# Optimization experiments

Hardware: AMD Instinct MI355X
Metric: run time of the kernel (lower is better)

## Reference

```python
import jax, jax.numpy as jnp
import numpy as np

T = 512        # seq_len
D = 128        # output_dim / trajectory feature dim
H_ENC = 512    # encoder hidden
H_DEC = 512    # decoder hidden
EMB = 256      # embedding size


def _lstm_step(h, c, x, Wi, Wh, bh):
    # flax LSTMCell: input dense has no bias, hidden dense has bias
    z = x @ Wi + h @ Wh + bh              # [4H]
    i, f, g, o = jnp.split(z, 4)
    i = jax.nn.sigmoid(i)
    f = jax.nn.sigmoid(f)
    g = jnp.tanh(g)
    o = jax.nn.sigmoid(o)
    c_new = f * c + i * g
    h_new = o * jnp.tanh(c_new)
    return h_new, c_new


def setup_inputs() -> dict:
    key = jax.random.key(0)
    ks = jax.random.split(key, 12)
    def w(k, shape, fan_in):
        return jax.random.normal(k, shape, dtype=jnp.float32) / np.sqrt(fan_in)
    return {
        "trajectory": jax.random.normal(ks[0], (T, D), dtype=jnp.float32),
        # encoder LSTM
        "enc_Wi": w(ks[1], (D, 4 * H_ENC), D),
        "enc_Wh": w(ks[2], (H_ENC, 4 * H_ENC), H_ENC),
        "enc_bh": jnp.zeros((4 * H_ENC,), jnp.float32),
        # encoder embedding projection
        "enc_emb_W": w(ks[3], (H_ENC, EMB), H_ENC),
        "enc_emb_b": jnp.zeros((EMB,), jnp.float32),
        # decoder initial-hidden projection from embedding
        "dec_init_W": w(ks[4], (EMB, H_DEC), EMB),
        "dec_init_b": jnp.zeros((H_DEC,), jnp.float32),
        # decoder LSTM
        "dec_Wi": w(ks[5], (D, 4 * H_DEC), D),
        "dec_Wh": w(ks[6], (H_DEC, 4 * H_DEC), H_DEC),
        "dec_bh": jnp.zeros((4 * H_DEC,), jnp.float32),
        # per-timestep decoder output Dense (fresh module each loop iter in original)
        "dec_out_W": w(ks[7], (T, H_DEC, D), H_DEC),
        "dec_out_b": jnp.zeros((T, D), jnp.float32),
    }


def reference(trajectory, enc_Wi, enc_Wh, enc_bh, enc_emb_W, enc_emb_b,
              dec_init_W, dec_init_b, dec_Wi, dec_Wh, dec_bh,
              dec_out_W, dec_out_b):
    # ---- Encoder: sequential LSTM over trajectory, zero init carry ----
    def enc_step(carry, x_t):
        h, c = carry
        h, c = _lstm_step(h, c, x_t, enc_Wi, enc_Wh, enc_bh)
        return (h, c), None
    h0 = jnp.zeros((H_ENC,), trajectory.dtype)
    c0 = jnp.zeros((H_ENC,), trajectory.dtype)
    (h, _), _ = jax.lax.scan(enc_step, (h0, c0), trajectory)
    embedding = h @ enc_emb_W + enc_emb_b  # [EMB]

    # per-timestep output Dense weights ----
    def dec_step(carry, wt):
        h, c, x = carry
        Wt, bt = wt
        h, c = _lstm_step(h, c, x, dec_Wi, dec_Wh, dec_bh)
        x = h @ Wt + bt  # flax LSTMCell output y == new h
        return (h, c, x), x
    hd0 = embedding @ dec_init_W + dec_init_b   # [H_DEC]
    cd0 = jnp.zeros((H_DEC,), trajectory.dtype)
    x0 = jnp.zeros((D,), trajectory.dtype)
    _, reconstruction = jax.lax.scan(dec_step, (hd0, cd0, x0), (dec_out_W, dec_out_b))
    return (reconstruction, embedding)
```

## Files before the change

kernel.cpp:

```cpp
#include <hip/hip_runtime.h>
#include <math.h>

#define T 512
#define D 128
#define H 512
#define EMB 256
#define Z4 2048
#define NWG 16
#define SLICE 32
#define NTH 512

typedef unsigned long long u64;
typedef unsigned int u32;

__device__ float g_xp[T * Z4];
__device__ u64 g_he[2][H];
__device__ u64 g_hd[2][H];
__device__ u64 g_xq[2][NWG][D];
__device__ float g_hd0[H];

__device__ __forceinline__ u64 aload64(const u64* p) {
    return __hip_atomic_load(p, __ATOMIC_RELAXED, __HIP_MEMORY_SCOPE_AGENT);
}
__device__ __forceinline__ void astore64(u64* p, u64 v) {
    __hip_atomic_store(p, v, __ATOMIC_RELAXED, __HIP_MEMORY_SCOPE_AGENT);
}
__device__ __forceinline__ u64 pack2(u32 tag, float v) {
    return ((u64)tag << 32) | (u64)__float_as_uint(v);
}
__device__ __forceinline__ float lo_f(u64 v) { return __uint_as_float((u32)v); }
__device__ __forceinline__ u32 hi_t(u64 v) { return (u32)(v >> 32); }
__device__ __forceinline__ float sigm(float x) { return 1.0f / (1.0f + expf(-x)); }

#define TT 16
__global__ __launch_bounds__(256, 1)
void k_xp(const float* __restrict__ traj, const float* __restrict__ Wi,
          const float* __restrict__ bh) {
    const int tid = threadIdx.x;
    if (blockIdx.y == 0) {
        const int fid = blockIdx.x * 256 + tid;
        if (fid < H) {
            g_he[0][fid] = 0ull; g_he[1][fid] = 0ull;
            g_hd[0][fid] = 0ull; g_hd[1][fid] = 0ull;
        }
        u64* xqf = &g_xq[0][0][0];
        xqf[fid] = 0ull; xqf[fid + 2048] = 0ull;
    }
    const int jc = blockIdx.x;
    const int t0 = blockIdx.y * TT;
    const int j  = jc * 256 + tid;

    __shared__ float tl[TT * D];
#pragma unroll
    for (int r = 0; r < (TT * D) / 256; ++r)
        tl[r * 256 + tid] = traj[t0 * D + r * 256 + tid];
    __syncthreads();

    float acc[TT];
#pragma unroll
    for (int tt = 0; tt < TT; ++tt) acc[tt] = 0.f;
    for (int i = 0; i < D; ++i) {
        const float wv = Wi[i * Z4 + j];
#pragma unroll
        for (int tt = 0; tt < TT; ++tt) acc[tt] += tl[tt * D + i] * wv;
    }
    const float bv = bh[j];
#pragma unroll
    for (int tt = 0; tt < TT; ++tt)
        g_xp[(t0 + tt) * Z4 + j] = acc[tt] + bv;
}

__global__ __launch_bounds__(NTH, 1)
void k_enc(const float* __restrict__ Wh) {
    const int w   = blockIdx.x;
    const int tid = threadIdx.x;
    const int jl  = tid & 127;
    const int p   = tid >> 7;
    const int k0  = w * SLICE;
    const int gcol = (jl >> 5) * H + k0 + (jl & 31);

    float wh[128];
#pragma unroll
    for (int q = 0; q < 128; ++q)
        wh[q] = Wh[(p * 128 + q) * Z4 + gcol];

    __shared__ float h_lds[H];
    __shared__ float zred[NTH];
    __shared__ float zfin[128];

    float creg = 0.f;

    for (int t = 0; t < T; ++t) {
        float xpv = (p == 0) ? g_xp[t * Z4 + gcol] : 0.f;

        if (t > 0) {
            const u32 want = (u32)t;
            u64 v;
            do { v = aload64(&g_he[t & 1][tid]); } while (hi_t(v) != want);
            h_lds[tid] = lo_f(v);
        } else {
            h_lds[tid] = 0.f;
        }
        __syncthreads();

        float acc = xpv;
#pragma unroll
        for (int q4 = 0; q4 < 32; ++q4) {
            const float4 hv = *reinterpret_cast<const float4*>(&h_lds[p * 128 + q4 * 4]);
            acc += hv.x * wh[q4 * 4 + 0] + hv.y * wh[q4 * 4 + 1] +
                   hv.z * wh[q4 * 4 + 2] + hv.w * wh[q4 * 4 + 3];
        }
        zred[tid] = acc;
        __syncthreads();
        if (tid < 128)
            zfin[tid] = zred[tid] + zred[128 + tid] + zred[256 + tid] + zred[384 + tid];
        __syncthreads();
        if (tid < SLICE) {
            const float zi = zfin[tid], zf = zfin[32 + tid],
                        zg = zfin[64 + tid], zo = zfin[96 + tid];
            const float cn = sigm(zf) * creg + sigm(zi) * tanhf(zg);
            creg = cn;
            const float hn = sigm(zo) * tanhf(cn);
            astore64(&g_he[(t + 1) & 1][k0 + tid], pack2((u32)(t + 1), hn));
        }
    }
}

__global__ __launch_bounds__(256, 1)
void k_emb(const float* __restrict__ embW, const float* __restrict__ embB,
           const float* __restrict__ diW, const float* __restrict__ diB,
           float* __restrict__ out) {
    const int tid = threadIdx.x;
    __shared__ float h_l[H];
    __shared__ float e_l[EMB];
#pragma unroll
    for (int r = 0; r < H / 256; ++r)
        h_l[r * 256 + tid] = lo_f(g_he[0][r * 256 + tid]);
    __syncthreads();

    float acc = embB[tid];
    for (int i = 0; i < H; ++i)
        acc += h_l[i] * embW[i * EMB + tid];
    e_l[tid] = acc;
    out[T * D + tid] = acc;
    __syncthreads();

#pragma unroll
    for (int r = 0; r < H / 256; ++r) {
        const int k = r * 256 + tid;
        float a2 = diB[k];
        for (int e = 0; e < EMB; ++e)
            a2 += e_l[e] * diW[e * H + k];
        g_hd0[k] = a2;
    }
}

__global__ __launch_bounds__(NTH, 1)
void k_dec(const float* __restrict__ Wi, const float* __restrict__ Wh,
           const float* __restrict__ bh, const float* __restrict__ Wt,
           const float* __restrict__ bt, float* __restrict__ out) {
    const int w   = blockIdx.x;
    const int tid = threadIdx.x;
    const int jl  = tid & 127;
    const int p   = tid >> 7;
    const int k0  = w * SLICE;
    const int gcol = (jl >> 5) * H + k0 + (jl & 31);
    const int d   = tid & 127;
    const int g4  = tid >> 7;

    float wx[32], wh[128];
#pragma unroll
    for (int q = 0; q < 32; ++q)
        wx[q] = Wi[(p * 32 + q) * Z4 + gcol];
#pragma unroll
    for (int q = 0; q < 128; ++q)
        wh[q] = Wh[(p * 128 + q) * Z4 + gcol];
    const float bhz = (tid < 128) ? bh[(tid >> 5) * H + k0 + (tid & 31)] : 0.f;

    __shared__ float h_lds[H];
    __shared__ float xs_lds[D];
    __shared__ float zred[NTH];
    __shared__ float zfin[128];
    __shared__ float hs_lds[SLICE];

    float creg = 0.f;

    for (int s = 0; s < T; ++s) {
        float wpre[SLICE];
        float btv = 0.f;
        if (tid < D) {
#pragma unroll
            for (int kk = 0; kk < SLICE; ++kk)
                wpre[kk] = Wt[((size_t)s * H + k0 + kk) * D + tid];
            if (w == 0) btv = bt[s * D + tid];
        }

        if (s > 0) {
            const u32 want = (u32)s;
            const int par  = s & 1;
            u64 vh, v0, v1, v2, v3;
            for (;;) {
                vh = aload64(&g_hd[par][tid]);
                v0 = aload64(&g_xq[par][g4 * 4 + 0][d]);
                v1 = aload64(&g_xq[par][g4 * 4 + 1][d]);
                v2 = aload64(&g_xq[par][g4 * 4 + 2][d]);
                v3 = aload64(&g_xq[par][g4 * 4 + 3][d]);
                if ((hi_t(vh) == want) & (hi_t(v0) == want) & (hi_t(v1) == want) &
                    (hi_t(v2) == want) & (hi_t(v3) == want)) break;
            }
            h_lds[tid] = lo_f(vh);
            zred[tid]  = lo_f(v0) + lo_f(v1) + lo_f(v2) + lo_f(v3);
            __syncthreads();
            if (tid < D) {
                const float xv = zred[tid] + zred[128 + tid] + zred[256 + tid] + zred[384 + tid];
                xs_lds[tid] = xv;
                if (w == 0) out[(size_t)(s - 1) * D + tid] = xv;
            }
        } else {
            h_lds[tid] = g_hd0[tid];
            if (tid < D) xs_lds[tid] = 0.f;
        }
        __syncthreads();

        float acc = 0.f;
#pragma unroll
        for (int q4 = 0; q4 < 8; ++q4) {
            const float4 xv = *reinterpret_cast<const float4*>(&xs_lds[p * 32 + q4 * 4]);
            acc += xv.x * wx[q4 * 4 + 0] + xv.y * wx[q4 * 4 + 1] +
                   xv.z * wx[q4 * 4 + 2] + xv.w * wx[q4 * 4 + 3];
        }
#pragma unroll
        for (int q4 = 0; q4 < 32; ++q4) {
            const float4 hv = *reinterpret_cast<const float4*>(&h_lds[p * 128 + q4 * 4]);
            acc += hv.x * wh[q4 * 4 + 0] + hv.y * wh[q4 * 4 + 1] +
                   hv.z * wh[q4 * 4 + 2] + hv.w * wh[q4 * 4 + 3];
        }
        zred[tid] = acc;
        __syncthreads();
        if (tid < 128)
            zfin[tid] = zred[tid] + zred[128 + tid] + zred[256 + tid] + zred[384 + tid] + bhz;
        __syncthreads();
        if (tid < SLICE) {
            const float zi = zfin[tid], zf = zfin[32 + tid],
                        zg = zfin[64 + tid], zo = zfin[96 + tid];
            const float cn = sigm(zf) * creg + sigm(zi) * tanhf(zg);
            creg = cn;
            const float hn = sigm(zo) * tanhf(cn);
            hs_lds[tid] = hn;
            astore64(&g_hd[(s + 1) & 1][k0 + tid], pack2((u32)(s + 1), hn));
        }
        __syncthreads();
        if (tid < D) {
            float px = btv;
#pragma unroll
            for (int kk = 0; kk < SLICE; ++kk)
                px += hs_lds[kk] * wpre[kk];
            astore64(&g_xq[(s + 1) & 1][w][tid], pack2((u32)(s + 1), px));
        }
    }

    if (w == 0) {
        const u32 want = (u32)T;
        u64 v0, v1, v2, v3;
        for (;;) {
            v0 = aload64(&g_xq[0][g4 * 4 + 0][d]);
            v1 = aload64(&g_xq[0][g4 * 4 + 1][d]);
            v2 = aload64(&g_xq[0][g4 * 4 + 2][d]);
            v3 = aload64(&g_xq[0][g4 * 4 + 3][d]);
            if ((hi_t(v0) == want) & (hi_t(v1) == want) &
                (hi_t(v2) == want) & (hi_t(v3) == want)) break;
        }
        zred[tid] = lo_f(v0) + lo_f(v1) + lo_f(v2) + lo_f(v3);
        __syncthreads();
        if (tid < D)
            out[(size_t)(T - 1) * D + tid] =
                zred[tid] + zred[128 + tid] + zred[256 + tid] + zred[384 + tid];
    }
}

extern "C" void kernel_launch(void* const* d_in, const int* in_sizes, int n_in,
                              void* d_out, int out_size, void* d_ws, size_t ws_size,
                              hipStream_t stream) {
    const float* traj  = (const float*)d_in[0];
    const float* encWi = (const float*)d_in[1];
    const float* encWh = (const float*)d_in[2];
    const float* encbh = (const float*)d_in[3];
    const float* embW  = (const float*)d_in[4];
    const float* embB  = (const float*)d_in[5];
    const float* diW   = (const float*)d_in[6];
    const float* diB   = (const float*)d_in[7];
    const float* decWi = (const float*)d_in[8];
    const float* decWh = (const float*)d_in[9];
    const float* decbh = (const float*)d_in[10];
    const float* doW   = (const float*)d_in[11];
    const float* dob   = (const float*)d_in[12];
    float* out = (float*)d_out;

    k_xp<<<dim3(8, T / TT), dim3(256), 0, stream>>>(traj, encWi, encbh);
    k_enc<<<dim3(NWG), dim3(NTH), 0, stream>>>(encWh);
    k_emb<<<dim3(1), dim3(256), 0, stream>>>(embW, embB, diW, diB, out);
    k_dec<<<dim3(NWG), dim3(NTH), 0, stream>>>(decWi, decWh, decbh, doW, dob, out);
}
```

Before: 2.818 ms.

## Replace LDS gate reductions with wave shuffles and overlap decoder x-poll with h matvec

The LSTM recurrent kernels now assign four adjacent lanes per gate column, so the partial dot products are reduced with xor-shuffles and the four gates are gathered by shuffles. This drops the zred/zfin LDS round trips and two barriers per step. The h buffer is double-buffered in LDS. The decoder waits on h first and computes the recurrent matvec before polling for the previous step's output x, so the x wait overlaps with work. Sigmoid and tanh use fast exp and rcp approximations, which trades a small amount of accuracy for latency.

```diff
diff --git a/kernel.cpp b/kernel.cpp
--- a/kernel.cpp
+++ b/kernel.cpp
@@ -30,7 +30,16 @@
 }
 __device__ __forceinline__ float lo_f(u64 v) { return __uint_as_float((u32)v); }
 __device__ __forceinline__ u32 hi_t(u64 v) { return (u32)(v >> 32); }
-__device__ __forceinline__ float sigm(float x) { return 1.0f / (1.0f + expf(-x)); }
+
+__device__ __forceinline__ float fsigm(float x) {
+    x = fminf(fmaxf(x, -30.f), 30.f);
+    return __builtin_amdgcn_rcpf(1.f + __expf(-x));
+}
+__device__ __forceinline__ float ftanh(float x) {
+    x = fminf(fmaxf(x, -15.f), 15.f);
+    const float e = __expf(2.f * x);
+    return (e - 1.f) * __builtin_amdgcn_rcpf(e + 1.f);
+}
 
 #define TT 16
 __global__ __launch_bounds__(256, 1)
@@ -70,59 +79,62 @@
         g_xp[(t0 + tt) * Z4 + j] = acc[tt] + bv;
 }
 
-__global__ __launch_bounds__(NTH, 1)
+
+__global__ __launch_bounds__(NTH, 2)
 void k_enc(const float* __restrict__ Wh) {
     const int w   = blockIdx.x;
     const int tid = threadIdx.x;
-    const int jl  = tid & 127;
-    const int p   = tid >> 7;
+    const int c   = tid >> 2;
+    const int p   = tid & 3;
+    const int u   = c >> 2;
+    const int gt  = c & 3;
     const int k0  = w * SLICE;
-    const int gcol = (jl >> 5) * H + k0 + (jl & 31);
+    const int col = gt * H + k0 + u;
+    const int l   = tid & 63;
+    const int lb  = (l & ~15) + (l & 3);
 
     float wh[128];
 #pragma unroll
     for (int q = 0; q < 128; ++q)
-        wh[q] = Wh[(p * 128 + q) * Z4 + gcol];
-
-    __shared__ float h_lds[H];
-    __shared__ float zred[NTH];
-    __shared__ float zfin[128];
+        wh[q] = Wh[(p * 128 + q) * Z4 + col];
+
+    __shared__ float hl[2][4][132];
 
     float creg = 0.f;
 
     for (int t = 0; t < T; ++t) {
-        float xpv = (p == 0) ? g_xp[t * Z4 + gcol] : 0.f;
+        const int par = t & 1;
+        float xpv = (p == 0) ? g_xp[t * Z4 + col] : 0.f;
 
         if (t > 0) {
             const u32 want = (u32)t;
-            u64 v;
-            do { v = aload64(&g_he[t & 1][tid]); } while (hi_t(v) != want);
-            h_lds[tid] = lo_f(v);
+            const u64* hp = &g_he[par][tid];
+            u64 a = aload64(hp);
+            for (;;) { u64 b = aload64(hp); if (hi_t(a) == want) break; a = b; }
+            hl[par][tid >> 7][tid & 127] = lo_f(a);
         } else {
-            h_lds[tid] = 0.f;
+            hl[par][tid >> 7][tid & 127] = 0.f;
         }
         __syncthreads();
 
         float acc = xpv;
 #pragma unroll
         for (int q4 = 0; q4 < 32; ++q4) {
-            const float4 hv = *reinterpret_cast<const float4*>(&h_lds[p * 128 + q4 * 4]);
+            const float4 hv = *reinterpret_cast<const float4*>(&hl[par][p][q4 * 4]);
             acc += hv.x * wh[q4 * 4 + 0] + hv.y * wh[q4 * 4 + 1] +
                    hv.z * wh[q4 * 4 + 2] + hv.w * wh[q4 * 4 + 3];
         }
-        zred[tid] = acc;
-        __syncthreads();
-        if (tid < 128)
-            zfin[tid] = zred[tid] + zred[128 + tid] + zred[256 + tid] + zred[384 + tid];
-        __syncthreads();
-        if (tid < SLICE) {
-            const float zi = zfin[tid], zf = zfin[32 + tid],
-                        zg = zfin[64 + tid], zo = zfin[96 + tid];
-            const float cn = sigm(zf) * creg + sigm(zi) * tanhf(zg);
-            creg = cn;
-            const float hn = sigm(zo) * tanhf(cn);
-            astore64(&g_he[(t + 1) & 1][k0 + tid], pack2((u32)(t + 1), hn));
-        }
+        acc += __shfl_xor(acc, 1);
+        acc += __shfl_xor(acc, 2);
+        const float zi = __shfl(acc, lb + 0);
+        const float zf = __shfl(acc, lb + 4);
+        const float zg = __shfl(acc, lb + 8);
+        const float zo = __shfl(acc, lb + 12);
+        const float cn = fsigm(zf) * creg + fsigm(zi) * ftanh(zg);
+        creg = cn;
+        const float hn = fsigm(zo) * ftanh(cn);
+        if ((tid & 15) == 0)
+            astore64(&g_he[(t + 1) & 1][k0 + (tid >> 4)], pack2((u32)(t + 1), hn));
     }
 }
 
@@ -155,99 +167,117 @@
     }
 }
 
-__global__ __launch_bounds__(NTH, 1)
+__global__ __launch_bounds__(NTH, 2)
 void k_dec(const float* __restrict__ Wi, const float* __restrict__ Wh,
            const float* __restrict__ bh, const float* __restrict__ Wt,
            const float* __restrict__ bt, float* __restrict__ out) {
     const int w   = blockIdx.x;
     const int tid = threadIdx.x;
-    const int jl  = tid & 127;
-    const int p   = tid >> 7;
+    const int c   = tid >> 2;
+    const int p   = tid & 3;
+    const int u   = c >> 2;
+    const int gt  = c & 3;
     const int k0  = w * SLICE;
-    const int gcol = (jl >> 5) * H + k0 + (jl & 31);
+    const int col = gt * H + k0 + u;
+    const int l   = tid & 63;
+    const int lb  = (l & ~15) + (l & 3);
     const int d   = tid & 127;
-    const int g4  = tid >> 7;
-
-    float wx[32], wh[128];
+    const int a4  = tid >> 7;
+
+    float wh[128], wx[32];
 #pragma unroll
     for (int q = 0; q < 32; ++q)
-        wx[q] = Wi[(p * 32 + q) * Z4 + gcol];
+        wx[q] = Wi[(p * 32 + q) * Z4 + col];
 #pragma unroll
     for (int q = 0; q < 128; ++q)
-        wh[q] = Wh[(p * 128 + q) * Z4 + gcol];
-    const float bhz = (tid < 128) ? bh[(tid >> 5) * H + k0 + (tid & 31)] : 0.f;
-
-    __shared__ float h_lds[H];
-    __shared__ float xs_lds[D];
-    __shared__ float zred[NTH];
-    __shared__ float zfin[128];
+        wh[q] = Wh[(p * 128 + q) * Z4 + col];
+    const float bhz = (p == 0) ? bh[col] : 0.f;
+
+    __shared__ float hl[2][4][132];
+    __shared__ float zxp[2][4][4][36];
     __shared__ float hs_lds[SLICE];
 
     float creg = 0.f;
 
     for (int s = 0; s < T; ++s) {
+        const int par = s & 1;
         float wpre[SLICE];
         float btv = 0.f;
         if (tid < D) {
 #pragma unroll
             for (int kk = 0; kk < SLICE; ++kk)
-                wpre[kk] = Wt[((size_t)s * H + k0 + kk) * D + tid];
-            if (w == 0) btv = bt[s * D + tid];
+                wpre[kk] = Wt[((size_t)s * H + k0 + kk) * D + d];
+            if (w == 0) btv = bt[s * D + d];
         }
 
         if (s > 0) {
             const u32 want = (u32)s;
-            const int par  = s & 1;
-            u64 vh, v0, v1, v2, v3;
+            const u64* hp = &g_hd[par][tid];
+            u64 a = aload64(hp);
+            for (;;) { u64 b = aload64(hp); if (hi_t(a) == want) break; a = b; }
+            hl[par][tid >> 7][tid & 127] = lo_f(a);
+        } else {
+            hl[par][tid >> 7][tid & 127] = g_hd0[tid];
+        }
+        __syncthreads();
+
+        float acc = bhz;
+#pragma unroll
+        for (int q4 = 0; q4 < 32; ++q4) {
+            const float4 hv = *reinterpret_cast<const float4*>(&hl[par][p][q4 * 4]);
+            acc += hv.x * wh[q4 * 4 + 0] + hv.y * wh[q4 * 4 + 1] +
+                   hv.z * wh[q4 * 4 + 2] + hv.w * wh[q4 * 4 + 3];
+        }
+
+        if (s > 0) {
+            const u32 want = (u32)s;
+            const u64* x0 = &g_xq[par][a4 * 4 + 0][d];
+            const u64* x1 = &g_xq[par][a4 * 4 + 1][d];
+            const u64* x2 = &g_xq[par][a4 * 4 + 2][d];
+            const u64* x3 = &g_xq[par][a4 * 4 + 3][d];
+            u64 v0, v1, v2, v3;
             for (;;) {
-                vh = aload64(&g_hd[par][tid]);
-                v0 = aload64(&g_xq[par][g4 * 4 + 0][d]);
-                v1 = aload64(&g_xq[par][g4 * 4 + 1][d]);
-                v2 = aload64(&g_xq[par][g4 * 4 + 2][d]);
-                v3 = aload64(&g_xq[par][g4 * 4 + 3][d]);
-                if ((hi_t(vh) == want) & (hi_t(v0) == want) & (hi_t(v1) == want) &
+                v0 = aload64(x0); v1 = aload64(x1);
+                v2 = aload64(x2); v3 = aload64(x3);
+                if ((hi_t(v0) == want) & (hi_t(v1) == want) &
                     (hi_t(v2) == want) & (hi_t(v3) == want)) break;
             }
-            h_lds[tid] = lo_f(vh);
-            zred[tid]  = lo_f(v0) + lo_f(v1) + lo_f(v2) + lo_f(v3);
-            __syncthreads();
-            if (tid < D) {
-                const float xv = zred[tid] + zred[128 + tid] + zred[256 + tid] + zred[384 + tid];
-                xs_lds[tid] = xv;
-                if (w == 0) out[(size_t)(s - 1) * D + tid] = xv;
+            zxp[par][a4][d >> 5][d & 31] = lo_f(v0) + lo_f(v1) + lo_f(v2) + lo_f(v3);
+        }
+        __syncthreads();
+
+        if (s > 0) {
+#pragma unroll
+            for (int q4 = 0; q4 < 8; ++q4) {
+                const float4 x0 = *reinterpret_cast<const float4*>(&zxp[par][0][p][q4 * 4]);
+                const float4 x1 = *reinterpret_cast<const float4*>(&zxp[par][1][p][q4 * 4]);
+                const float4 x2 = *reinterpret_cast<const float4*>(&zxp[par][2][p][q4 * 4]);
+                const float4 x3 = *reinterpret_cast<const float4*>(&zxp[par][3][p][q4 * 4]);
+                const float sx = x0.x + x1.x + x2.x + x3.x;
+                const float sy = x0.y + x1.y + x2.y + x3.y;
+                const float sz = x0.z + x1.z + x2.z + x3.z;
+                const float sw = x0.w + x1.w + x2.w + x3.w;
+                acc += sx * wx[q4 * 4 + 0] + sy * wx[q4 * 4 + 1] +
+                       sz * wx[q4 * 4 + 2] + sw * wx[q4 * 4 + 3];
             }
-        } else {
-            h_lds[tid] = g_hd0[tid];
-            if (tid < D) xs_lds[tid] = 0.f;
-        }
-        __syncthreads();
-
-        float acc = 0.f;
-#pragma unroll
-        for (int q4 = 0; q4 < 8; ++q4) {
-            const float4 xv = *reinterpret_cast<const float4*>(&xs_lds[p * 32 + q4 * 4]);
-            acc += xv.x * wx[q4 * 4 + 0] + xv.y * wx[q4 * 4 + 1] +
-                   xv.z * wx[q4 * 4 + 2] + xv.w * wx[q4 * 4 + 3];
-        }
-#pragma unroll
-        for (int q4 = 0; q4 < 32; ++q4) {
-            const float4 hv = *reinterpret_cast<const float4*>(&h_lds[p * 128 + q4 * 4]);
-            acc += hv.x * wh[q4 * 4 + 0] + hv.y * wh[q4 * 4 + 1] +
-                   hv.z * wh[q4 * 4 + 2] + hv.w * wh[q4 * 4 + 3];
-        }
-        zred[tid] = acc;
-        __syncthreads();
-        if (tid < 128)
-            zfin[tid] = zred[tid] + zred[128 + tid] + zred[256 + tid] + zred[384 + tid] + bhz;
-        __syncthreads();
-        if (tid < SLICE) {
-            const float zi = zfin[tid], zf = zfin[32 + tid],
-                        zg = zfin[64 + tid], zo = zfin[96 + tid];
-            const float cn = sigm(zf) * creg + sigm(zi) * tanhf(zg);
-            creg = cn;
-            const float hn = sigm(zo) * tanhf(cn);
-            hs_lds[tid] = hn;
-            astore64(&g_hd[(s + 1) & 1][k0 + tid], pack2((u32)(s + 1), hn));
+            if (w == 0 && tid < D)
+                out[(size_t)(s - 1) * D + d] =
+                    zxp[par][0][d >> 5][d & 31] + zxp[par][1][d >> 5][d & 31] +
+                    zxp[par][2][d >> 5][d & 31] + zxp[par][3][d >> 5][d & 31];
+        }
+
+        acc += __shfl_xor(acc, 1);
+        acc += __shfl_xor(acc, 2);
+        const float zi = __shfl(acc, lb + 0);
+        const float zf = __shfl(acc, lb + 4);
+        const float zg = __shfl(acc, lb + 8);
+        const float zo = __shfl(acc, lb + 12);
+        const float cn = fsigm(zf) * creg + fsigm(zi) * ftanh(zg);
+        creg = cn;
+        const float hn = fsigm(zo) * ftanh(cn);
+        if ((tid & 15) == 0) {
+            hs_lds[tid >> 4] = hn;
+            astore64(&g_hd[(s + 1) & 1][k0 + (tid >> 4)], pack2((u32)(s + 1), hn));
         }
         __syncthreads();
         if (tid < D) {
@@ -255,7 +285,7 @@
 #pragma unroll
             for (int kk = 0; kk < SLICE; ++kk)
                 px += hs_lds[kk] * wpre[kk];
-            astore64(&g_xq[(s + 1) & 1][w][tid], pack2((u32)(s + 1), px));
+            astore64(&g_xq[(s + 1) & 1][w][d], pack2((u32)(s + 1), px));
         }
     }
 
@@ -263,18 +293,19 @@
         const u32 want = (u32)T;
         u64 v0, v1, v2, v3;
         for (;;) {
-            v0 = aload64(&g_xq[0][g4 * 4 + 0][d]);
-            v1 = aload64(&g_xq[0][g4 * 4 + 1][d]);
-            v2 = aload64(&g_xq[0][g4 * 4 + 2][d]);
-            v3 = aload64(&g_xq[0][g4 * 4 + 3][d]);
+            v0 = aload64(&g_xq[0][a4 * 4 + 0][d]);
+            v1 = aload64(&g_xq[0][a4 * 4 + 1][d]);
+            v2 = aload64(&g_xq[0][a4 * 4 + 2][d]);
+            v3 = aload64(&g_xq[0][a4 * 4 + 3][d]);
             if ((hi_t(v0) == want) & (hi_t(v1) == want) &
                 (hi_t(v2) == want) & (hi_t(v3) == want)) break;
         }
-        zred[tid] = lo_f(v0) + lo_f(v1) + lo_f(v2) + lo_f(v3);
+        zxp[0][a4][d >> 5][d & 31] = lo_f(v0) + lo_f(v1) + lo_f(v2) + lo_f(v3);
         __syncthreads();
         if (tid < D)
-            out[(size_t)(T - 1) * D + tid] =
-                zred[tid] + zred[128 + tid] + zred[256 + tid] + zred[384 + tid];
+            out[(size_t)(T - 1) * D + d] =
+                zxp[0][0][d >> 5][d & 31] + zxp[0][1][d >> 5][d & 31] +
+                zxp[0][2][d >> 5][d & 31] + zxp[0][3][d >> 5][d & 31];
     }
 }
 
```

New measurement: 7.014 ms. +148.9%, slower.
